# Kernel tuning notes

Measured on AMD Instinct MI355X. Metric: run time of the kernel, lower is better.

Reference implementation:

```python
import jax, jax.numpy as jnp
import numpy as np


def setup_inputs() -> dict:
    key = jax.random.key(0)
    k1, k2, k3, k4 = jax.random.split(key, 4)
    B, T, H, A = 32, 2048, 1024, 512
    enc_dim = 2 * H
    return {
        "encoder_feature": jax.random.normal(k1, (B, T, enc_dim), dtype=jnp.float32),
        "decoder_state": jax.random.normal(k2, (B, H), dtype=jnp.float32),
        "attention_mask": jnp.ones((B, 1, T), dtype=jnp.float32),
        "Wq": jax.random.normal(k3, (A, H), dtype=jnp.float32) * (1.0 / np.sqrt(H)),
        "bq": jnp.zeros((A,), dtype=jnp.float32),
        "Wk": jax.random.normal(k4, (A, enc_dim), dtype=jnp.float32) * (1.0 / np.sqrt(enc_dim)),
        "bk": jnp.zeros((A,), dtype=jnp.float32),
    }


def reference(encoder_feature, decoder_state, attention_mask, Wq, bq, Wk, bk):
    # key: relu(per-time linear)  [B, T, A]
    key = jax.nn.relu(jnp.einsum("bte,ae->bta", encoder_feature, Wk) + bk)
    # query: relu(linear)  [B, A]
    query = jax.nn.relu(decoder_state @ Wq.T + bq)
    # energy = bmm(query[B,1,A], key^T[B,A,T]) -> [B,1,T]
    energy = jnp.einsum("ba,bta->bt", query, key)[:, None, :]
    attention = jax.nn.softmax(energy, axis=-1)
    attention = attention * attention_mask
    attention = attention / jnp.sum(attention, axis=-1, keepdims=True)
    # context = bmm(attention[B,1,T], enc[B,T,E]) -> squeeze -> [B, E]
    context = jnp.einsum("bt,bte->be", attention[:, 0, :], encoder_feature)
    return (attention, context)
```

## Files before the change

kernel.cpp:

```cpp
#include <hip/hip_runtime.h>
#include <math.h>

constexpr int Bn = 32;
constexpr int Tn = 2048;
constexpr int Hn = 1024;
constexpr int An = 512;
constexpr int En = 2048;

typedef __attribute__((ext_vector_type(8))) _Float16 halfx8;
typedef __attribute__((ext_vector_type(4))) float floatx4;

constexpr float WK_SCALE = 4096.0f;
constexpr float WK_INV   = 1.0f / 4096.0f;

__device__ __forceinline__ unsigned short f2h_bits(float x) {
  _Float16 h = (_Float16)x;
  return __builtin_bit_cast(unsigned short, h);
}

__device__ __forceinline__ void gload_lds16(const void* g, void* lds) {
  __builtin_amdgcn_global_load_lds(
      (const __attribute__((address_space(1))) unsigned int*)g,
      (__attribute__((address_space(3))) unsigned int*)lds, 16, 0, 0);
}

__global__ void wk_prep(const float* __restrict__ Wk,
                        unsigned short* __restrict__ wkh,
                        unsigned short* __restrict__ wkl) {
  const int lin = blockIdx.x * 256 + threadIdx.x;
  float4 v = ((const float4*)Wk)[lin];
  ushort4 h, l;
  float s, hf;
  s = v.x * WK_SCALE; h.x = f2h_bits(s); hf = (float)__builtin_bit_cast(_Float16, h.x); l.x = f2h_bits(s - hf);
  s = v.y * WK_SCALE; h.y = f2h_bits(s); hf = (float)__builtin_bit_cast(_Float16, h.y); l.y = f2h_bits(s - hf);
  s = v.z * WK_SCALE; h.z = f2h_bits(s); hf = (float)__builtin_bit_cast(_Float16, h.z); l.z = f2h_bits(s - hf);
  s = v.w * WK_SCALE; h.w = f2h_bits(s); hf = (float)__builtin_bit_cast(_Float16, h.w); l.w = f2h_bits(s - hf);
  ((ushort4*)wkh)[lin] = h;
  ((ushort4*)wkl)[lin] = l;
}

__global__ void query_kernel(const float* __restrict__ dec,
                             const float* __restrict__ Wq,
                             const float* __restrict__ bq,
                             float* __restrict__ qbuf,
                             float* __restrict__ energy_zero) {
  __shared__ float sdec[Hn];
  const int b = blockIdx.x;
  const int gl = (blockIdx.y * 32 + blockIdx.x) * 128 + threadIdx.x;
  ((float4*)energy_zero)[gl] = make_float4(0.f, 0.f, 0.f, 0.f);

  for (int i = threadIdx.x; i < Hn; i += blockDim.x) sdec[i] = dec[b * Hn + i];
  __syncthreads();
  const int a = blockIdx.y * 128 + threadIdx.x;
  const float* w = Wq + (size_t)a * Hn;
  float acc = 0.f;
  #pragma unroll 4
  for (int k = 0; k < Hn; k += 4) {
    float4 wv = *(const float4*)(w + k);
    acc = fmaf(wv.x, sdec[k + 0], acc);
    acc = fmaf(wv.y, sdec[k + 1], acc);
    acc = fmaf(wv.z, sdec[k + 2], acc);
    acc = fmaf(wv.w, sdec[k + 3], acc);
  }
  qbuf[b * An + a] = fmaxf(acc + bq[a], 0.f);
}

__global__ __launch_bounds__(256, 2)
void energy_kernel(const float* __restrict__ enc,
                   const unsigned short* __restrict__ wkh,
                   const unsigned short* __restrict__ wkl,
                   const float* __restrict__ bk,
                   const float* __restrict__ qbuf,
                   float* __restrict__ energy) {
  __shared__ unsigned short sA[128 * 64];
  __shared__ unsigned short sBh[256 * 64];
  __shared__ unsigned short sBl[256 * 64];

  const int tid = threadIdx.x;
  const int lane = tid & 63;
  const int wid = tid >> 6;
  const int wr = wid >> 1, wc = wid & 1;
  const int lr = lane & 15, lq = lane >> 4;

  const int nblk = blockIdx.x & 1;
  const long row_base = (long)(blockIdx.x >> 1) * 128;
  const int n_base = nblk * 256;
  const int b = (int)(row_base >> 11);

  floatx4 acc[4][8];
  #pragma unroll
  for (int i = 0; i < 4; ++i)
    #pragma unroll
    for (int j = 0; j < 8; ++j) acc[i][j] = (floatx4){0.f, 0.f, 0.f, 0.f};

  for (int k0 = 0; k0 < En; k0 += 64) {
    #pragma unroll
    for (int rep = 0; rep < 8; ++rep) {
      const int lin = tid + rep * 256;
      const int row = lin >> 4, e4 = lin & 15;
      float4 v = *(const float4*)(enc + (row_base + row) * En + k0 + e4 * 4);
      ushort4 h;
      h.x = f2h_bits(v.x); h.y = f2h_bits(v.y);
      h.z = f2h_bits(v.z); h.w = f2h_bits(v.w);
      const int chunk = e4 >> 1, half = e4 & 1;
      const int off = row * 64 + ((chunk ^ (row & 7)) << 3) + (half << 2);
      *(ushort4*)&sA[off] = h;
    }
    #pragma unroll
    for (int it = 0; it < 8; ++it) {
      const int gidx = wid * 512 + it * 64 + lane;
      const int a = gidx >> 3;
      const int c = (gidx & 7) ^ (a & 7);
      const size_t goff = (size_t)(n_base + a) * En + k0 + c * 8;
      unsigned short* ldsb_h = &sBh[(wid * 512 + it * 64) * 8];
      unsigned short* ldsb_l = &sBl[(wid * 512 + it * 64) * 8];
      gload_lds16(wkh + goff, ldsb_h);
      gload_lds16(wkl + goff, ldsb_l);
    }
    __syncthreads();

    #pragma unroll
    for (int ks = 0; ks < 2; ++ks) {
      const int cb = ks * 4 + lq;
      halfx8 ah[4];
      #pragma unroll
      for (int mt = 0; mt < 4; ++mt) {
        const int m = wr * 64 + mt * 16 + lr;
        ah[mt] = *(const halfx8*)&sA[m * 64 + ((cb ^ (m & 7)) << 3)];
      }
      #pragma unroll
      for (int ng = 0; ng < 2; ++ng) {
        halfx8 bh[4], bl[4];
        #pragma unroll
        for (int nt = 0; nt < 4; ++nt) {
          const int n = wc * 128 + (ng * 4 + nt) * 16 + lr;
          const int off = n * 64 + ((cb ^ (n & 7)) << 3);
          bh[nt] = *(const halfx8*)&sBh[off];
          bl[nt] = *(const halfx8*)&sBl[off];
        }
        #pragma unroll
        for (int mt = 0; mt < 4; ++mt)
          #pragma unroll
          for (int nt = 0; nt < 4; ++nt) {
            acc[mt][ng * 4 + nt] = __builtin_amdgcn_mfma_f32_16x16x32_f16(ah[mt], bl[nt], acc[mt][ng * 4 + nt], 0, 0, 0);
            acc[mt][ng * 4 + nt] = __builtin_amdgcn_mfma_f32_16x16x32_f16(ah[mt], bh[nt], acc[mt][ng * 4 + nt], 0, 0, 0);
          }
      }
    }
    __syncthreads();
  }

  float bkv[8], qv[8];
  #pragma unroll
  for (int nt = 0; nt < 8; ++nt) {
    const int ncol = n_base + wc * 128 + nt * 16 + lr;
    bkv[nt] = bk[ncol];
    qv[nt] = qbuf[b * An + ncol];
  }
  #pragma unroll
  for (int mt = 0; mt < 4; ++mt) {
    #pragma unroll
    for (int r = 0; r < 4; ++r) {
      float s = 0.f;
      #pragma unroll
      for (int nt = 0; nt < 8; ++nt)
        s = fmaf(fmaxf(fmaf(acc[mt][nt][r], WK_INV, bkv[nt]), 0.f), qv[nt], s);
      s += __shfl_xor(s, 1, 64);
      s += __shfl_xor(s, 2, 64);
      s += __shfl_xor(s, 4, 64);
      s += __shfl_xor(s, 8, 64);
      if (lr == 0) {
        const long row = row_base + wr * 64 + mt * 16 + lq * 4 + r;
        atomicAdd(&energy[row], s);
      }
    }
  }
}

__global__ void softmax_kernel(float* __restrict__ att,
                               const float* __restrict__ mask,
                               uint2* __restrict__ list,
                               unsigned* __restrict__ cnt) {
  const int b = blockIdx.x;
  const int tid = threadIdx.x;
  const int lane = tid & 63;
  const int wave = tid >> 6;
  __shared__ float wred[4];
  __shared__ unsigned cnt_l;
  if (tid == 0) cnt_l = 0;

  float e[8];
  float m = -INFINITY;
  #pragma unroll
  for (int i = 0; i < 8; ++i) {
    e[i] = att[b * Tn + tid + i * 256];
    m = fmaxf(m, e[i]);
  }
  #pragma unroll
  for (int off = 32; off > 0; off >>= 1) m = fmaxf(m, __shfl_xor(m, off, 64));
  if (lane == 0) wred[wave] = m;
  __syncthreads();
  m = fmaxf(fmaxf(wred[0], wred[1]), fmaxf(wred[2], wred[3]));
  __syncthreads();

  float p[8];
  float s = 0.f;
  #pragma unroll
  for (int i = 0; i < 8; ++i) {
    p[i] = expf(e[i] - m) * mask[b * Tn + tid + i * 256];
    s += p[i];
  }
  #pragma unroll
  for (int off = 32; off > 0; off >>= 1) s += __shfl_xor(s, off, 64);
  if (lane == 0) wred[wave] = s;
  __syncthreads();
  const float inv = 1.f / (wred[0] + wred[1] + wred[2] + wred[3]);
  #pragma unroll
  for (int i = 0; i < 8; ++i) {
    const int t = tid + i * 256;
    const float w = p[i] * inv;
    att[b * Tn + t] = w;
    if (w > 1e-7f) {
      unsigned pos = atomicAdd(&cnt_l, 1u);
      list[b * Tn + pos] = make_uint2((unsigned)t, __float_as_uint(w));
    }
  }
  __syncthreads();
  if (tid == 0) cnt[b] = cnt_l;
}

__global__ void context_kernel(const float* __restrict__ enc,
                               const uint2* __restrict__ list,
                               const unsigned* __restrict__ cnt,
                               float* __restrict__ ctx) {
  const int ec = blockIdx.x, b = blockIdx.y;
  const int tid = threadIdx.x;
  __shared__ uint2 slist[Tn];
  const int n = (int)cnt[b];
  for (int j = tid; j < n; j += 256) slist[j] = list[b * Tn + j];
  __syncthreads();

  const int e0 = ec * 1024 + tid * 4;
  const float* base = enc + (size_t)b * Tn * En + e0;
  float4 a0 = make_float4(0, 0, 0, 0), a1 = a0, a2 = a0, a3 = a0;
  int j = 0;
  for (; j + 4 <= n; j += 4) {
    uint2 p0 = slist[j], p1 = slist[j + 1], p2 = slist[j + 2], p3 = slist[j + 3];
    float4 v0 = *(const float4*)(base + (size_t)p0.x * En);
    float4 v1 = *(const float4*)(base + (size_t)p1.x * En);
    float4 v2 = *(const float4*)(base + (size_t)p2.x * En);
    float4 v3 = *(const float4*)(base + (size_t)p3.x * En);
    const float w0 = __uint_as_float(p0.y), w1 = __uint_as_float(p1.y);
    const float w2 = __uint_as_float(p2.y), w3 = __uint_as_float(p3.y);
    a0.x = fmaf(w0, v0.x, a0.x); a0.y = fmaf(w0, v0.y, a0.y); a0.z = fmaf(w0, v0.z, a0.z); a0.w = fmaf(w0, v0.w, a0.w);
    a1.x = fmaf(w1, v1.x, a1.x); a1.y = fmaf(w1, v1.y, a1.y); a1.z = fmaf(w1, v1.z, a1.z); a1.w = fmaf(w1, v1.w, a1.w);
    a2.x = fmaf(w2, v2.x, a2.x); a2.y = fmaf(w2, v2.y, a2.y); a2.z = fmaf(w2, v2.z, a2.z); a2.w = fmaf(w2, v2.w, a2.w);
    a3.x = fmaf(w3, v3.x, a3.x); a3.y = fmaf(w3, v3.y, a3.y); a3.z = fmaf(w3, v3.z, a3.z); a3.w = fmaf(w3, v3.w, a3.w);
  }
  for (; j < n; ++j) {
    uint2 p0 = slist[j];
    float4 v0 = *(const float4*)(base + (size_t)p0.x * En);
    const float w0 = __uint_as_float(p0.y);
    a0.x = fmaf(w0, v0.x, a0.x); a0.y = fmaf(w0, v0.y, a0.y); a0.z = fmaf(w0, v0.z, a0.z); a0.w = fmaf(w0, v0.w, a0.w);
  }
  a0.x += a1.x + a2.x + a3.x; a0.y += a1.y + a2.y + a3.y;
  a0.z += a1.z + a2.z + a3.z; a0.w += a1.w + a2.w + a3.w;
  *(float4*)(ctx + b * En + e0) = a0;
}

extern "C" void kernel_launch(void* const* d_in, const int* in_sizes, int n_in,
                              void* d_out, int out_size, void* d_ws, size_t ws_size,
                              hipStream_t stream) {
  const float* enc  = (const float*)d_in[0];
  const float* dec  = (const float*)d_in[1];
  const float* mask = (const float*)d_in[2];
  const float* Wq   = (const float*)d_in[3];
  const float* bq   = (const float*)d_in[4];
  const float* Wk   = (const float*)d_in[5];
  const float* bk   = (const float*)d_in[6];

  float* out = (float*)d_out;
  float* att = out;
  float* ctx = out + Bn * Tn;

  unsigned short* wkh = (unsigned short*)d_ws;
  unsigned short* wkl = wkh + (size_t)An * En;
  float* qbuf = (float*)(wkl + (size_t)An * En);
  unsigned* cnt = (unsigned*)(qbuf + Bn * An);
  uint2* list = (uint2*)(cnt + 32);

  wk_prep<<<(An * En) / (256 * 4), 256, 0, stream>>>(Wk, wkh, wkl);
  query_kernel<<<dim3(Bn, 4), 128, 0, stream>>>(dec, Wq, bq, qbuf, att);
  energy_kernel<<<(Bn * Tn / 128) * 2, 256, 0, stream>>>(enc, wkh, wkl, bk, qbuf, att);
  softmax_kernel<<<Bn, 256, 0, stream>>>(att, mask, list, cnt);
  context_kernel<<<dim3(2, Bn), 256, 0, stream>>>(enc, list, cnt, ctx);
}
```

Before: 873.3 us.

## Shrink energy GEMM N-tile to 128, remap blocks per XCD, split query dot

The energy GEMM's N tile drops from 256 to 128 columns, so each 128-row slab of the encoder is now converted and loaded by four blocks instead of two. This halves the accumulator and LDS footprint, which allows three blocks per CU instead of two. Block IDs are remapped so the four N-blocks of one row slab land on the same XCD, aiming for L2 reuse of the encoder tile. The query kernel splits each dot product across 4 lanes with a shuffle reduce, raising parallelism. The cost is twice the global reads and fp16 conversion of the encoder tile, plus more atomics into energy.

After: 891.9 us. +2.1%, slower.

```diff
diff --git a/kernel.cpp b/kernel.cpp
--- a/kernel.cpp
+++ b/kernel.cpp
@@ -39,33 +39,39 @@
   ((ushort4*)wkl)[lin] = l;
 }
 
-__global__ void query_kernel(const float* __restrict__ dec,
-                             const float* __restrict__ Wq,
-                             const float* __restrict__ bq,
-                             float* __restrict__ qbuf,
-                             float* __restrict__ energy_zero) {
+__global__ __launch_bounds__(256)
+void query_kernel(const float* __restrict__ dec,
+                  const float* __restrict__ Wq,
+                  const float* __restrict__ bq,
+                  float* __restrict__ qbuf,
+                  float* __restrict__ energy_zero) {
   __shared__ float sdec[Hn];
   const int b = blockIdx.x;
-  const int gl = (blockIdx.y * 32 + blockIdx.x) * 128 + threadIdx.x;
-  ((float4*)energy_zero)[gl] = make_float4(0.f, 0.f, 0.f, 0.f);
-
-  for (int i = threadIdx.x; i < Hn; i += blockDim.x) sdec[i] = dec[b * Hn + i];
-  __syncthreads();
-  const int a = blockIdx.y * 128 + threadIdx.x;
-  const float* w = Wq + (size_t)a * Hn;
+  const int ag = blockIdx.y;
+  const int tid = threadIdx.x;
+  energy_zero[(blockIdx.y * 32 + blockIdx.x) * 256 + tid] = 0.f;
+
+  for (int i = tid; i < Hn; i += 256) sdec[i] = dec[b * Hn + i];
+  __syncthreads();
+  const int a = ag * 64 + (tid >> 2);
+  const int kq = tid & 3;
+  const float* w = Wq + (size_t)a * Hn + kq * 256;
+  const float* sd = sdec + kq * 256;
   float acc = 0.f;
   #pragma unroll 4
-  for (int k = 0; k < Hn; k += 4) {
+  for (int k = 0; k < 256; k += 4) {
     float4 wv = *(const float4*)(w + k);
-    acc = fmaf(wv.x, sdec[k + 0], acc);
-    acc = fmaf(wv.y, sdec[k + 1], acc);
-    acc = fmaf(wv.z, sdec[k + 2], acc);
-    acc = fmaf(wv.w, sdec[k + 3], acc);
-  }
-  qbuf[b * An + a] = fmaxf(acc + bq[a], 0.f);
-}
-
-__global__ __launch_bounds__(256, 2)
+    acc = fmaf(wv.x, sd[k + 0], acc);
+    acc = fmaf(wv.y, sd[k + 1], acc);
+    acc = fmaf(wv.z, sd[k + 2], acc);
+    acc = fmaf(wv.w, sd[k + 3], acc);
+  }
+  acc += __shfl_xor(acc, 1, 64);
+  acc += __shfl_xor(acc, 2, 64);
+  if (kq == 0) qbuf[b * An + a] = fmaxf(acc + bq[a], 0.f);
+}
+
+__global__ __launch_bounds__(256, 3)
 void energy_kernel(const float* __restrict__ enc,
                    const unsigned short* __restrict__ wkh,
                    const unsigned short* __restrict__ wkl,
@@ -73,8 +79,8 @@
                    const float* __restrict__ qbuf,
                    float* __restrict__ energy) {
   __shared__ unsigned short sA[128 * 64];
-  __shared__ unsigned short sBh[256 * 64];
-  __shared__ unsigned short sBl[256 * 64];
+  __shared__ unsigned short sBh[128 * 64];
+  __shared__ unsigned short sBl[128 * 64];
 
   const int tid = threadIdx.x;
   const int lane = tid & 63;
@@ -82,16 +88,20 @@
   const int wr = wid >> 1, wc = wid & 1;
   const int lr = lane & 15, lq = lane >> 4;
 
-  const int nblk = blockIdx.x & 1;
-  const long row_base = (long)(blockIdx.x >> 1) * 128;
-  const int n_base = nblk * 256;
-  const int b = (int)(row_base >> 11);
-
-  floatx4 acc[4][8];
+  const int bid = blockIdx.x;
+  const int xcd = bid & 7;
+  const int rem = bid >> 3;
+  const int nblk = rem & 3;
+  const int g = (rem >> 2) * 8 + xcd;
+  const long row_base = (long)g * 128;
+  const int n_base = nblk * 128;
+  const int b = g >> 4;
+
+  floatx4 acc[4][4];
   #pragma unroll
   for (int i = 0; i < 4; ++i)
     #pragma unroll
-    for (int j = 0; j < 8; ++j) acc[i][j] = (floatx4){0.f, 0.f, 0.f, 0.f};
+    for (int j = 0; j < 4; ++j) acc[i][j] = (floatx4){0.f, 0.f, 0.f, 0.f};
 
   for (int k0 = 0; k0 < En; k0 += 64) {
     #pragma unroll
@@ -107,15 +117,13 @@
       *(ushort4*)&sA[off] = h;
     }
     #pragma unroll
-    for (int it = 0; it < 8; ++it) {
-      const int gidx = wid * 512 + it * 64 + lane;
+    for (int it = 0; it < 4; ++it) {
+      const int gidx = wid * 256 + it * 64 + lane;
       const int a = gidx >> 3;
       const int c = (gidx & 7) ^ (a & 7);
       const size_t goff = (size_t)(n_base + a) * En + k0 + c * 8;
-      unsigned short* ldsb_h = &sBh[(wid * 512 + it * 64) * 8];
-      unsigned short* ldsb_l = &sBl[(wid * 512 + it * 64) * 8];
-      gload_lds16(wkh + goff, ldsb_h);
-      gload_lds16(wkl + goff, ldsb_l);
+      gload_lds16(wkh + goff, &sBh[(wid * 256 + it * 64) * 8]);
+      gload_lds16(wkl + goff, &sBl[(wid * 256 + it * 64) * 8]);
     }
     __syncthreads();
 
@@ -128,32 +136,29 @@
         const int m = wr * 64 + mt * 16 + lr;
         ah[mt] = *(const halfx8*)&sA[m * 64 + ((cb ^ (m & 7)) << 3)];
       }
+      halfx8 bh[4], bl[4];
       #pragma unroll
-      for (int ng = 0; ng < 2; ++ng) {
-        halfx8 bh[4], bl[4];
+      for (int nt = 0; nt < 4; ++nt) {
+        const int n = wc * 64 + nt * 16 + lr;
+        const int off = n * 64 + ((cb ^ (n & 7)) << 3);
+        bh[nt] = *(const halfx8*)&sBh[off];
+        bl[nt] = *(const halfx8*)&sBl[off];
+      }
+      #pragma unroll
+      for (int mt = 0; mt < 4; ++mt)
         #pragma unroll
         for (int nt = 0; nt < 4; ++nt) {
-          const int n = wc * 128 + (ng * 4 + nt) * 16 + lr;
-          const int off = n * 64 + ((cb ^ (n & 7)) << 3);
-          bh[nt] = *(const halfx8*)&sBh[off];
-          bl[nt] = *(const halfx8*)&sBl[off];
+          acc[mt][nt] = __builtin_amdgcn_mfma_f32_16x16x32_f16(ah[mt], bl[nt], acc[mt][nt], 0, 0, 0);
+          acc[mt][nt] = __builtin_amdgcn_mfma_f32_16x16x32_f16(ah[mt], bh[nt], acc[mt][nt], 0, 0, 0);
         }
-        #pragma unroll
-        for (int mt = 0; mt < 4; ++mt)
-          #pragma unroll
-          for (int nt = 0; nt < 4; ++nt) {
-            acc[mt][ng * 4 + nt] = __builtin_amdgcn_mfma_f32_16x16x32_f16(ah[mt], bl[nt], acc[mt][ng * 4 + nt], 0, 0, 0);
-            acc[mt][ng * 4 + nt] = __builtin_amdgcn_mfma_f32_16x16x32_f16(ah[mt], bh[nt], acc[mt][ng * 4 + nt], 0, 0, 0);
-          }
-      }
     }
     __syncthreads();
   }
 
-  float bkv[8], qv[8];
-  #pragma unroll
-  for (int nt = 0; nt < 8; ++nt) {
-    const int ncol = n_base + wc * 128 + nt * 16 + lr;
+  float bkv[4], qv[4];
+  #pragma unroll
+  for (int nt = 0; nt < 4; ++nt) {
+    const int ncol = n_base + wc * 64 + nt * 16 + lr;
     bkv[nt] = bk[ncol];
     qv[nt] = qbuf[b * An + ncol];
   }
@@ -163,7 +168,7 @@
     for (int r = 0; r < 4; ++r) {
       float s = 0.f;
       #pragma unroll
-      for (int nt = 0; nt < 8; ++nt)
+      for (int nt = 0; nt < 4; ++nt)
         s = fmaf(fmaxf(fmaf(acc[mt][nt][r], WK_INV, bkv[nt]), 0.f), qv[nt], s);
       s += __shfl_xor(s, 1, 64);
       s += __shfl_xor(s, 2, 64);
@@ -290,8 +295,8 @@
   uint2* list = (uint2*)(cnt + 32);
 
   wk_prep<<<(An * En) / (256 * 4), 256, 0, stream>>>(Wk, wkh, wkl);
-  query_kernel<<<dim3(Bn, 4), 128, 0, stream>>>(dec, Wq, bq, qbuf, att);
-  energy_kernel<<<(Bn * Tn / 128) * 2, 256, 0, stream>>>(enc, wkh, wkl, bk, qbuf, att);
+  query_kernel<<<dim3(Bn, 8), 256, 0, stream>>>(dec, Wq, bq, qbuf, att);
+  energy_kernel<<<(Bn * Tn / 128) * 4, 256, 0, stream>>>(enc, wkh, wkl, bk, qbuf, att);
   softmax_kernel<<<Bn, 256, 0, stream>>>(att, mask, list, cnt);
   context_kernel<<<dim3(2, Bn), 256, 0, stream>>>(enc, list, cnt, ctx);
 }
```
